# Performance work log

Hardware: AMD Instinct MI355X
Metric: run time of the kernel (lower is better)

## Reference

```python
import jax, jax.numpy as jnp
from jax import lax
import numpy as np

B, T, D_IN, H = 4096, 64, 300, 3


def setup_inputs() -> dict:
    key = jax.random.key(0)
    k_x, k_len, k_wih, k_whh, k_bih, k_bhh = jax.random.split(key, 6)
    x = jax.random.normal(k_x, (B, T, D_IN), dtype=jnp.float32)
    lengths = jax.random.randint(k_len, (B,), 1, T + 1, dtype=jnp.int64)
    # PyTorch nn.RNN init: uniform(-1/sqrt(H), 1/sqrt(H))
    bound = 1.0 / np.sqrt(H)
    W_ih = jax.random.uniform(k_wih, (H, D_IN), jnp.float32, -bound, bound)
    W_hh = jax.random.uniform(k_whh, (H, H), jnp.float32, -bound, bound)
    b_ih = jax.random.uniform(k_bih, (H,), jnp.float32, -bound, bound)
    b_hh = jax.random.uniform(k_bhh, (H,), jnp.float32, -bound, bound)
    return {"x": x, "lengths": lengths, "W_ih": W_ih, "W_hh": W_hh,
            "b_ih": b_ih, "b_hh": b_hh}


def reference(x, lengths, W_ih, W_hh, b_ih, b_hh):
    # Tanh RNN over packed variable-length sequences. The packed RNN returns
    # hidden = h at step lengths[i]-1 for each sample i; we emulate packing
    # with a masked scan: h only updates while t < lengths[i].
    Bn, Tn, _ = x.shape
    # Hoist the input projection into one big GEMM: [B,T,H]
    xb = jnp.einsum('bti,hi->bth', x, W_ih) + b_ih
    mask = jnp.arange(Tn)[None, :] < lengths[:, None]  # [B,T] bool

    def step(h, inp):
        xt, m = inp  # xt: [B,H], m: [B,1]
        h_new = jnp.tanh(xt + h @ W_hh.T + b_hh)
        return jnp.where(m, h_new, h), None

    h0 = jnp.zeros((Bn, W_hh.shape[0]), dtype=x.dtype)
    h_last, _ = lax.scan(step, h0,
                         (xb.transpose(1, 0, 2), mask.T[:, :, None]))
    return h_last  # [B, H] == hidden.squeeze(0)
```

## Files before the change

### kernel.cpp

```cpp
#include <hip/hip_runtime.h>
#include <math.h>

#define B_ 4096
#define T_ 64
#define DIN_ 300
#define H_ 3
#define NF4 75

__device__ __forceinline__ float fast_tanh(float x) {
  float xc = fminf(fmaxf(x, -9.0f), 9.0f);
  float t = __expf(2.0f * xc);
  return (t - 1.0f) * __builtin_amdgcn_rcpf(t + 1.0f);
}

__global__ __launch_bounds__(256) void rnn_fused_kernel(
    const float* __restrict__ x,
    const int* __restrict__ lraw,
    const float* __restrict__ W_ih,
    const float* __restrict__ W_hh,
    const float* __restrict__ b_ih,
    const float* __restrict__ b_hh,
    float* __restrict__ out) {
  const int b = blockIdx.x;
  const int tid = threadIdx.x;

  __shared__ float4 Wl[H_][76];
  __shared__ float4 xb_s[T_];

  if (tid < H_ * NF4) {
    int h = tid / NF4;
    int i = tid - h * NF4;
    Wl[h][i] = reinterpret_cast<const float4*>(W_ih)[h * NF4 + i];
  }

  const bool is32 = (lraw[1] != 0);
  int L = is32 ? lraw[b] : lraw[2 * b];
  if (L < 1) L = 1;
  if (L > T_) L = T_;
  __syncthreads();

  const int wave = tid >> 6;
  const int lane = tid & 63;
  const int g = lane >> 2;
  const int s = lane & 3;
  const int row = wave * 16 + g;

  if (wave * 16 < L) {
    const bool rowok = (row < L);
    const float4* xr = reinterpret_cast<const float4*>(
        x + (size_t)b * (T_ * DIN_) + (size_t)row * DIN_);

    float a0 = 0.f, a1 = 0.f, a2 = 0.f;
#pragma unroll 4
    for (int k = 0; k < 19; ++k) {
      int idx = 4 * k + s;
      if (rowok && idx < NF4) {
        float4 v = xr[idx];
        float4 w0 = Wl[0][idx];
        float4 w1 = Wl[1][idx];
        float4 w2 = Wl[2][idx];
        a0 += v.x * w0.x + v.y * w0.y + v.z * w0.z + v.w * w0.w;
        a1 += v.x * w1.x + v.y * w1.y + v.z * w1.z + v.w * w1.w;
        a2 += v.x * w2.x + v.y * w2.y + v.z * w2.z + v.w * w2.w;
      }
    }
    a0 += __shfl_xor(a0, 1);
    a1 += __shfl_xor(a1, 1);
    a2 += __shfl_xor(a2, 1);
    a0 += __shfl_xor(a0, 2);
    a1 += __shfl_xor(a1, 2);
    a2 += __shfl_xor(a2, 2);
    if (s == 0 && rowok) xb_s[row] = make_float4(a0, a1, a2, 0.f);
  }
  __syncthreads();

  if (tid != 0) return;

  const float w00 = W_hh[0], w01 = W_hh[1], w02 = W_hh[2];
  const float w10 = W_hh[3], w11 = W_hh[4], w12 = W_hh[5];
  const float w20 = W_hh[6], w21 = W_hh[7], w22 = W_hh[8];
  const float c0 = b_ih[0] + b_hh[0];
  const float c1 = b_ih[1] + b_hh[1];
  const float c2 = b_ih[2] + b_hh[2];
  float h0 = 0.f, h1 = 0.f, h2 = 0.f;
  float4 cur = xb_s[0];
  for (int t = 0; t < L; ++t) {
    float4 nxt = xb_s[(t + 1 < L) ? t + 1 : t];
    float a0 = cur.x + c0 + w00 * h0 + w01 * h1 + w02 * h2;
    float a1 = cur.y + c1 + w10 * h0 + w11 * h1 + w12 * h2;
    float a2 = cur.z + c2 + w20 * h0 + w21 * h1 + w22 * h2;
    h0 = fast_tanh(a0);
    h1 = fast_tanh(a1);
    h2 = fast_tanh(a2);
    cur = nxt;
  }
  out[b * 3 + 0] = h0;
  out[b * 3 + 1] = h1;
  out[b * 3 + 2] = h2;
}

extern "C" void kernel_launch(void* const* d_in, const int* in_sizes, int n_in,
                              void* d_out, int out_size, void* d_ws,
                              size_t ws_size, hipStream_t stream) {
  const float* x = (const float*)d_in[0];
  const int* lraw = (const int*)d_in[1];
  const float* W_ih = (const float*)d_in[2];
  const float* W_hh = (const float*)d_in[3];
  const float* b_ih = (const float*)d_in[4];
  const float* b_hh = (const float*)d_in[5];
  float* out = (float*)d_out;

  rnn_fused_kernel<<<B_, 256, 0, stream>>>(x, lraw, W_ih, W_hh, b_ih, b_hh,
                                           out);
}
```

Measured before the change: 414.2 us.

## Keep W_ih in registers and map 16 lanes per row for coalesced loads

Drops the shared-memory staging of W_ih and its barrier. Each lane now holds its slice of the weights in registers, loaded directly from global memory. The projection uses 16 lanes per timestep row instead of 4, so each warp reads contiguous 256-byte chunks of a row. Rows are spread across waves in a strided loop, so only waves with valid rows do work. This adds register pressure of 15 float4 weights plus 5 x vectors per lane, and needs two more shuffle stages in the reduction.

```diff
diff --git a/kernel.cpp b/kernel.cpp
--- a/kernel.cpp
+++ b/kernel.cpp
@@ -23,53 +23,56 @@
     float* __restrict__ out) {
   const int b = blockIdx.x;
   const int tid = threadIdx.x;
+  const int wave = tid >> 6;
+  const int lane = tid & 63;
+  const int grp = lane >> 4;
+  const int s = lane & 15;
 
-  __shared__ float4 Wl[H_][76];
   __shared__ float4 xb_s[T_];
-
-  if (tid < H_ * NF4) {
-    int h = tid / NF4;
-    int i = tid - h * NF4;
-    Wl[h][i] = reinterpret_cast<const float4*>(W_ih)[h * NF4 + i];
-  }
 
   const bool is32 = (lraw[1] != 0);
   int L = is32 ? lraw[b] : lraw[2 * b];
   if (L < 1) L = 1;
   if (L > T_) L = T_;
-  __syncthreads();
 
-  const int wave = tid >> 6;
-  const int lane = tid & 63;
-  const int g = lane >> 2;
-  const int s = lane & 3;
-  const int row = wave * 16 + g;
+  const float4* W4 = reinterpret_cast<const float4*>(W_ih);
+  float4 w[H_][5];
+#pragma unroll
+  for (int h = 0; h < H_; ++h) {
+#pragma unroll
+    for (int k = 0; k < 4; ++k) w[h][k] = W4[h * NF4 + 16 * k + s];
+    w[h][4] = (s < 11) ? W4[h * NF4 + 64 + s]
+                       : make_float4(0.f, 0.f, 0.f, 0.f);
+  }
 
-  if (wave * 16 < L) {
+  const float* xbase = x + (size_t)b * (T_ * DIN_);
+  for (int base = wave * 4; base < L; base += 16) {
+    const int row = base + grp;
     const bool rowok = (row < L);
-    const float4* xr = reinterpret_cast<const float4*>(
-        x + (size_t)b * (T_ * DIN_) + (size_t)row * DIN_);
-
+    const float4* xr =
+        reinterpret_cast<const float4*>(xbase + (size_t)row * DIN_);
     float a0 = 0.f, a1 = 0.f, a2 = 0.f;
-#pragma unroll 4
-    for (int k = 0; k < 19; ++k) {
-      int idx = 4 * k + s;
-      if (rowok && idx < NF4) {
-        float4 v = xr[idx];
-        float4 w0 = Wl[0][idx];
-        float4 w1 = Wl[1][idx];
-        float4 w2 = Wl[2][idx];
-        a0 += v.x * w0.x + v.y * w0.y + v.z * w0.z + v.w * w0.w;
-        a1 += v.x * w1.x + v.y * w1.y + v.z * w1.z + v.w * w1.w;
-        a2 += v.x * w2.x + v.y * w2.y + v.z * w2.z + v.w * w2.w;
+    if (rowok) {
+      float4 v[5];
+#pragma unroll
+      for (int k = 0; k < 4; ++k) v[k] = xr[16 * k + s];
+      v[4] = (s < 11) ? xr[64 + s] : make_float4(0.f, 0.f, 0.f, 0.f);
+#pragma unroll
+      for (int k = 0; k < 5; ++k) {
+        a0 += v[k].x * w[0][k].x + v[k].y * w[0][k].y + v[k].z * w[0][k].z +
+              v[k].w * w[0][k].w;
+        a1 += v[k].x * w[1][k].x + v[k].y * w[1][k].y + v[k].z * w[1][k].z +
+              v[k].w * w[1][k].w;
+        a2 += v[k].x * w[2][k].x + v[k].y * w[2][k].y + v[k].z * w[2][k].z +
+              v[k].w * w[2][k].w;
       }
     }
-    a0 += __shfl_xor(a0, 1);
-    a1 += __shfl_xor(a1, 1);
-    a2 += __shfl_xor(a2, 1);
-    a0 += __shfl_xor(a0, 2);
-    a1 += __shfl_xor(a1, 2);
-    a2 += __shfl_xor(a2, 2);
+#pragma unroll
+    for (int off = 1; off <= 8; off <<= 1) {
+      a0 += __shfl_xor(a0, off);
+      a1 += __shfl_xor(a1, off);
+      a2 += __shfl_xor(a2, off);
+    }
     if (s == 0 && rowok) xb_s[row] = make_float4(a0, a1, a2, 0.f);
   }
   __syncthreads();
```

New measurement: 400.4 us. 3.3% less time.
